# Optimization experiments

Hardware: AMD Instinct MI355X
Metric: run time of the kernel (lower is better)

The kernel has to match this reference:

```python
import jax, jax.numpy as jnp
import numpy as np

N_ATOMS = 16384
N_EDGES = 65536
ATOM_DIM = 29
BOND_DIM = 8
UNITS = 64          # message_units / embed_dim
STEPS = 4
HEADS = 8
DENSE = 512
B_MOL = 256         # molecules
T_ATOMS = 64        # atoms per molecule (N_ATOMS = B_MOL * T_ATOMS)


def setup_inputs() -> dict:
    key = jax.random.key(0)
    ks = jax.random.split(key, 24)
    D = UNITS

    atom_features = jax.random.normal(ks[0], (N_ATOMS, ATOM_DIM), jnp.float32)
    bond_features = jax.random.normal(ks[1], (N_EDGES, BOND_DIM), jnp.float32)
    # edges within molecules
    mol = jax.random.randint(ks[2], (N_EDGES,), 0, B_MOL)
    a = jax.random.randint(ks[3], (N_EDGES,), 0, T_ATOMS)
    b = jax.random.randint(ks[4], (N_EDGES,), 0, T_ATOMS)
    pair_indices = jnp.stack([mol * T_ATOMS + a, mol * T_ATOMS + b], axis=1).astype(jnp.int32)
    molecule_indicator = (jnp.arange(N_ATOMS) // T_ATOMS).astype(jnp.int32)

    def xavier(k, shape, fan_in):
        return jax.random.normal(k, shape, jnp.float32) * (1.0 / np.sqrt(fan_in))

    params = dict(
        kernel=xavier(ks[5], (BOND_DIM, D * D), BOND_DIM),
        kernel_bias=jnp.zeros((D * D,), jnp.float32),
        gru_w_ih=xavier(ks[6], (3 * D, D), D),
        gru_w_hh=xavier(ks[7], (3 * D, D), D),
        gru_b_ih=jnp.zeros((3 * D,), jnp.float32),
        gru_b_hh=jnp.zeros((3 * D,), jnp.float32),
        in_proj_w=xavier(ks[8], (3 * D, D), D),
        in_proj_b=jnp.zeros((3 * D,), jnp.float32),
        out_proj_w=xavier(ks[9], (D, D), D),
        out_proj_b=jnp.zeros((D,), jnp.float32),
        ffn_w1=xavier(ks[10], (D, DENSE), D),
        ffn_b1=jnp.zeros((DENSE,), jnp.float32),
        ffn_w2=xavier(ks[11], (DENSE, D), DENSE),
        ffn_b2=jnp.zeros((D,), jnp.float32),
        ln1_g=jnp.ones((D,), jnp.float32),
        ln1_b=jnp.zeros((D,), jnp.float32),
        ln2_g=jnp.ones((D,), jnp.float32),
        ln2_b=jnp.zeros((D,), jnp.float32),
        d1_w=xavier(ks[12], (D, DENSE), D),
        d1_b=jnp.zeros((DENSE,), jnp.float32),
        d2_w=xavier(ks[13], (DENSE, 1), DENSE),
        d2_b=jnp.zeros((1,), jnp.float32),
    )
    return dict(atom_features=atom_features, bond_features=bond_features,
                pair_indices=pair_indices, molecule_indicator=molecule_indicator, **params)


def _layernorm(x, g, b, eps=1e-5):
    mu = x.mean(-1, keepdims=True)
    var = ((x - mu) ** 2).mean(-1, keepdims=True)
    return (x - mu) * jax.lax.rsqrt(var + eps) * g + b


def _forward(atom_features, bond_features, pair_indices, molecule_indicator,
             kernel, kernel_bias, gru_w_ih, gru_w_hh, gru_b_ih, gru_b_hh,
             in_proj_w, in_proj_b, out_proj_w, out_proj_b,
             ffn_w1, ffn_b1, ffn_w2, ffn_b2, ln1_g, ln1_b, ln2_g, ln2_b,
             d1_w, d1_b, d2_w, d2_b):
    D = UNITS
    n = atom_features.shape[0]
    # pad atom features to message_units
    h = jnp.pad(atom_features, ((0, 0), (0, D - atom_features.shape[1])))

    src = pair_indices[:, 0]
    dst = pair_indices[:, 1]
    # per-edge bond-conditioned transform matrices: [E, D, D]
    bond_mat = (bond_features @ kernel + kernel_bias).reshape(-1, D, D)

    for _ in range(STEPS):
        nbr = h[dst]                                      # gather [E, D]
        msg = jnp.einsum('eij,ej->ei', bond_mat, nbr)     # per-edge matvec
        agg = jax.ops.segment_sum(msg, src, num_segments=n)  # scatter-add [N, D]
        # GRUCell(input=agg, hidden=h)
        gi = agg @ gru_w_ih.T + gru_b_ih
        gh = h @ gru_w_hh.T + gru_b_hh
        i_r, i_z, i_n = jnp.split(gi, 3, axis=-1)
        h_r, h_z, h_n = jnp.split(gh, 3, axis=-1)
        r = jax.nn.sigmoid(i_r + h_r)
        z = jax.nn.sigmoid(i_z + h_z)
        nn_ = jnp.tanh(i_n + r * h_n)
        h = (1.0 - z) * nn_ + z * h

    # PartitionPadding: scatter atoms into [B_MOL, T_ATOMS, D] (indicator sorted, contiguous)
    starts = jnp.searchsorted(molecule_indicator, jnp.arange(B_MOL, dtype=molecule_indicator.dtype))
    pos = jnp.arange(n) - starts[molecule_indicator]
    x = jnp.zeros((B_MOL, T_ATOMS, D), h.dtype).at[molecule_indicator, pos].set(h)

    valid = jnp.any(x != 0, axis=-1)                      # [B, T] key-padding mask

    # multi-head self-attention
    qkv = x @ in_proj_w.T + in_proj_b                     # [B, T, 3D]
    q, k, v = jnp.split(qkv, 3, axis=-1)
    hd = D // HEADS
    q = q.reshape(B_MOL, T_ATOMS, HEADS, hd)
    k = k.reshape(B_MOL, T_ATOMS, HEADS, hd)
    v = v.reshape(B_MOL, T_ATOMS, HEADS, hd)
    scores = jnp.einsum('bqhd,bkhd->bhqk', q, k) / np.sqrt(hd)
    scores = jnp.where(valid[:, None, None, :], scores, -1e9)
    attn = jax.nn.softmax(scores, axis=-1)
    ao = jnp.einsum('bhqk,bkhd->bqhd', attn, v).reshape(B_MOL, T_ATOMS, D)
    ao = ao @ out_proj_w.T + out_proj_b

    y1 = _layernorm(x + ao, ln1_g, ln1_b)
    ffn = jax.nn.relu(y1 @ ffn_w1 + ffn_b1) @ ffn_w2 + ffn_b2
    y2 = _layernorm(y1 + ffn, ln2_g, ln2_b)
    pooled = y2.mean(axis=1)                              # [B, D]

    out = jax.nn.relu(pooled @ d1_w + d1_b)
    return jax.nn.sigmoid(out @ d2_w + d2_b)              # [B, 1]


def reference(atom_features, bond_features, pair_indices, molecule_indicator,
              kernel, kernel_bias, gru_w_ih, gru_w_hh, gru_b_ih, gru_b_hh,
              in_proj_w, in_proj_b, out_proj_w, out_proj_b,
              ffn_w1, ffn_b1, ffn_w2, ffn_b2, ln1_g, ln1_b, ln2_g, ln2_b,
              d1_w, d1_b, d2_w, d2_b):
    return _forward(atom_features, bond_features, pair_indices, molecule_indicator,
                    kernel, kernel_bias, gru_w_ih, gru_w_hh, gru_b_ih, gru_b_hh,
                    in_proj_w, in_proj_b, out_proj_w, out_proj_b,
                    ffn_w1, ffn_b1, ffn_w2, ffn_b2, ln1_g, ln1_b, ln2_g, ln2_b,
                    d1_w, d1_b, d2_w, d2_b)
```

## Files before the change

kernel.cpp:

```cpp
#include <hip/hip_runtime.h>
#include <hip/hip_bf16.h>
#include <math.h>

#define NA 16384
#define NE 65536
#define AD 29

typedef __attribute__((ext_vector_type(8))) short bfrag8;
typedef __attribute__((ext_vector_type(4))) float f32x4;

__device__ __forceinline__ float sigmoidf_(float x) { return 1.0f / (1.0f + expf(-x)); }
__device__ __forceinline__ unsigned short bf16bits(float x) {
  __hip_bfloat16 hb = __float2bfloat16(x);
  return *reinterpret_cast<unsigned short*>(&hb);
}
__device__ __forceinline__ float bf16val(unsigned short u) {
  unsigned int b = ((unsigned int)u) << 16;
  return __uint_as_float(b);
}

__global__ void k_init_prep(
    const float* __restrict__ af, float* __restrict__ h, int* __restrict__ count,
    const float* __restrict__ kern, const float* __restrict__ kbias,
    const float* __restrict__ wih, const float* __restrict__ whh,
    const float* __restrict__ w1, const float* __restrict__ w2,
    const float* __restrict__ ipw, const float* __restrict__ opw,
    unsigned short* __restrict__ KrA,
    unsigned short* __restrict__ Wh, unsigned short* __restrict__ Wl,
    unsigned short* __restrict__ W1h, unsigned short* __restrict__ W1l,
    unsigned short* __restrict__ W2h, unsigned short* __restrict__ W2l,
    unsigned short* __restrict__ PQh, unsigned short* __restrict__ PQl,
    unsigned short* __restrict__ POh, unsigned short* __restrict__ POl) {
  int idx0 = blockIdx.x * 256 + threadIdx.x;
  if (idx0 >= NA * 64) return;
  if (idx0 < NA) count[idx0] = 0;
  {
    int a = idx0 >> 6, d = idx0 & 63;
    h[idx0] = (d < AD) ? af[a * AD + d] : 0.0f;
  }
  if (idx0 < 36864) {
    int idx = idx0;
    int r = idx & 7;
    int lane = (idx >> 3) & 63;
    int tmp2 = idx >> 9;
    int ks = tmp2 % 18, w = tmp2 / 18;
    int i = w * 16 + (lane & 15);
    int kj = ks * 32 + ((lane >> 4) << 3) + r;
    int k9 = kj >> 6, j = kj & 63;
    float v = (k9 < 8) ? kern[k9 * 4096 + i * 64 + j] : kbias[i * 64 + j];
    KrA[idx] = bf16bits(v);
  } else if (idx0 < 61440) {
    int idx = idx0 - 36864;
    int r = idx & 7;
    int lane = (idx >> 3) & 63;
    int t2 = idx >> 9;
    int ks = t2 & 1;
    int t3 = t2 >> 1;
    int q = t3 % 6, w = t3 / 6;
    int s = q / 3, g = q % 3;
    int R = g * 64 + w * 16 + (lane & 15);
    int kk = ks * 32 + ((lane >> 4) << 3) + r;
    float v = (s == 0) ? wih[R * 64 + kk] : whh[R * 64 + kk];
    unsigned short hi = bf16bits(v);
    Wh[idx] = hi;
    Wl[idx] = bf16bits(v - bf16val(hi));
  } else if (idx0 < 126976) {
    int idx = idx0 - 61440;
    int r = idx & 7;
    int lane = (idx >> 3) & 63;
    int rest = (idx >> 9) & 63;
    if (idx < 32768) {
      int tile = rest >> 1, ks = rest & 1;
      int hid = tile * 16 + (lane & 15);
      int kk = ks * 32 + ((lane >> 4) << 3) + r;
      float v = w1[kk * 512 + hid];
      unsigned short hi = bf16bits(v);
      W1h[idx] = hi;
      W1l[idx] = bf16bits(v - bf16val(hi));
    } else {
      int i2 = idx - 32768;
      int tile = rest >> 4, ks = rest & 15;
      int outr = tile * 16 + (lane & 15);
      int kk = ks * 32 + ((lane >> 4) << 3) + r;
      float v = w2[kk * 64 + outr];
      unsigned short hi = bf16bits(v);
      W2h[i2] = hi;
      W2l[i2] = bf16bits(v - bf16val(hi));
    }
  } else if (idx0 < 143360) {
    int i = idx0 - 126976;
    if (i < 12288) {
      int r = i & 7;
      int lane = (i >> 3) & 63;
      int rest = i >> 9;
      int t = rest >> 1, ks = rest & 1;
      int R = t * 16 + (lane & 15);
      int kk = ks * 32 + ((lane >> 4) << 3) + r;
      float v = ipw[R * 64 + kk];
      unsigned short hi = bf16bits(v);
      PQh[i] = hi;
      PQl[i] = bf16bits(v - bf16val(hi));
    } else {
      int i2 = i - 12288;
      int r = i2 & 7;
      int lane = (i2 >> 3) & 63;
      int rest = i2 >> 9;
      int t = rest >> 1, ks = rest & 1;
      int R = t * 16 + (lane & 15);
      int kk = ks * 32 + ((lane >> 4) << 3) + r;
      float v = opw[R * 64 + kk];
      unsigned short hi = bf16bits(v);
      POh[i2] = hi;
      POl[i2] = bf16bits(v - bf16val(hi));
    }
  }
}

__global__ void k_count(const int* __restrict__ pairs, int* __restrict__ count) {
  int e = blockIdx.x * 256 + threadIdx.x;
  if (e >= NE) return;
  atomicAdd(&count[pairs[2 * e]], 1);
}
__global__ void k_scan1(const int* __restrict__ count, int* __restrict__ bsum) {
  __shared__ int red[256];
  int b = blockIdx.x, t = threadIdx.x;
  red[t] = count[b * 256 + t];
  __syncthreads();
  for (int s = 128; s > 0; s >>= 1) { if (t < s) red[t] += red[t + s]; __syncthreads(); }
  if (t == 0) bsum[b] = red[0];
}
__global__ void k_scan2(const int* __restrict__ count, const int* __restrict__ bsum,
                        int* __restrict__ start, int* __restrict__ cursor) {
  __shared__ int sc[256];
  __shared__ int basev;
  int b = blockIdx.x, t = threadIdx.x;
  if (t < 64) {
    int v = (t < b) ? bsum[t] : 0;
#pragma unroll
    for (int off = 1; off < 64; off <<= 1) v += __shfl_xor(v, off, 64);
    if (t == 0) basev = v;
  }
  int v = count[b * 256 + t];
  sc[t] = v;
  __syncthreads();
  for (int off = 1; off < 256; off <<= 1) {
    int add = (t >= off) ? sc[t - off] : 0;
    __syncthreads();
    sc[t] += add;
    __syncthreads();
  }
  int excl = sc[t] - v + basev;
  start[b * 256 + t] = excl;
  cursor[b * 256 + t] = excl;
  if (b * 256 + t == NA - 1) start[NA] = excl + v;
}
__global__ void k_place(const int* __restrict__ pairs, int* __restrict__ cursor,
                        const float* __restrict__ bf, int* __restrict__ sdst,
                        float* __restrict__ sbf) {
  int e = blockIdx.x * 256 + threadIdx.x;
  if (e >= NE) return;
  int src = pairs[2 * e], dst = pairs[2 * e + 1];
  int pos = atomicAdd(&cursor[src], 1);
  sdst[pos] = dst;
  const float4* b4 = reinterpret_cast<const float4*>(&bf[e * 8]);
  float4* s4 = reinterpret_cast<float4*>(&sbf[(size_t)pos * 8]);
  s4[0] = b4[0];
  s4[1] = b4[1];
}

#define MW 4
#define MAW 4
__global__ __launch_bounds__(256, 5) void k_msg(
    const float* __restrict__ h_in, const int* __restrict__ start,
    const int* __restrict__ sdst, const float* __restrict__ sbf,
    const unsigned short* __restrict__ KrA,
    const unsigned short* __restrict__ Wh, const unsigned short* __restrict__ Wl,
    const float* __restrict__ bih, const float* __restrict__ bhh,
    float* __restrict__ h_out) {
  __shared__ __align__(16) unsigned short Tb[16 * 584];
  __shared__ __align__(16) unsigned short Xh[16 * 136];
  __shared__ __align__(16) unsigned short Xl[16 * 136];
  __shared__ __align__(16) float Hf[16 * 68];
  float* AHa = reinterpret_cast<float*>(Tb);
  const int tid = threadIdx.x, lane = tid & 63, wv = tid >> 6;
  const int ablk = blockIdx.x * 16;
  const int awave = ablk + wv * MAW;

#pragma unroll
  for (int aa = 0; aa < MAW; ++aa) {
    const int a = wv * MAW + aa;
    const float v = h_in[(ablk + a) * 64 + lane];
    Hf[a * 68 + lane] = v;
    const unsigned short hi = bf16bits(v);
    Xh[a * 136 + 64 + lane] = hi;
    Xl[a * 136 + 64 + lane] = bf16bits(v - bf16val(hi));
  }

  int s0[MAW], s1[MAW];
#pragma unroll
  for (int a = 0; a < MAW; ++a) {
    s0[a] = __builtin_amdgcn_readfirstlane(start[awave + a]);
    s1[a] = __builtin_amdgcn_readfirstlane(start[awave + a + 1]);
  }
  float t[MAW][9];
#pragma unroll
  for (int a = 0; a < MAW; ++a)
#pragma unroll
    for (int k = 0; k < 9; ++k) t[a][k] = 0.f;

  float hv[MAW][8];
#pragma unroll
  for (int a = 0; a < MAW; ++a) {
    const int cnt = s1[a] - s0[a];
#pragma unroll
    for (int i = 0; i < 8; ++i) {
      hv[a][i] = 0.f;
      if (i < cnt) {
        int d = sdst[s0[a] + i];
        hv[a][i] = h_in[d * 64 + lane];
      }
    }
  }
#pragma unroll
  for (int a = 0; a < MAW; ++a) {
    const int cnt = s1[a] - s0[a];
#pragma unroll
    for (int i = 0; i < 8; ++i) {
      if (i < cnt) {
#pragma unroll
        for (int k = 0; k < 8; ++k)
          t[a][k] = fmaf(sbf[(size_t)(s0[a] + i) * 8 + k], hv[a][i], t[a][k]);
        t[a][8] += hv[a][i];
      }
    }
  }
#pragma unroll
  for (int a = 0; a < MAW; ++a) {
    for (int base = s0[a] + 8; base < s1[a]; base += 8) {
      const int nb = s1[a] - base;
      float hv2[8];
#pragma unroll
      for (int i = 0; i < 8; ++i) {
        hv2[i] = 0.f;
        if (i < nb) {
          int d = sdst[base + i];
          hv2[i] = h_in[d * 64 + lane];
        }
      }
#pragma unroll
      for (int i = 0; i < 8; ++i) {
        if (i < nb) {
#pragma unroll
          for (int k = 0; k < 8; ++k)
            t[a][k] = fmaf(sbf[(size_t)(base + i) * 8 + k], hv2[i], t[a][k]);
          t[a][8] += hv2[i];
        }
      }
    }
  }
#pragma unroll
  for (int a = 0; a < MAW; ++a) {
    const int row = wv * MAW + a;
#pragma unroll
    for (int k = 0; k < 9; ++k) Tb[row * 584 + k * 64 + lane] = bf16bits(t[a][k]);
  }
  __syncthreads();

  f32x4 acc = {0.f, 0.f, 0.f, 0.f};
  const bfrag8* KrA8 = reinterpret_cast<const bfrag8*>(KrA);
  const int tb_base = (lane & 15) * 584 + ((lane >> 4) << 3);
#pragma unroll 3
  for (int ks = 0; ks < 18; ++ks) {
    bfrag8 af = KrA8[(wv * 18 + ks) * 64 + lane];
    bfrag8 bfr = *reinterpret_cast<const bfrag8*>(&Tb[tb_base + ks * 32]);
    acc = __builtin_amdgcn_mfma_f32_16x16x32_bf16(af, bfr, acc, 0, 0, 0);
  }
#pragma unroll
  for (int reg = 0; reg < 4; ++reg) {
    const int ii = wv * 16 + ((lane >> 4) << 2) + reg;
    const unsigned short hi = bf16bits(acc[reg]);
    Xh[(lane & 15) * 136 + ii] = hi;
    Xl[(lane & 15) * 136 + ii] = bf16bits(acc[reg] - bf16val(hi));
  }
  __syncthreads();

  const bfrag8* Wh8 = reinterpret_cast<const bfrag8*>(Wh);
  const bfrag8* Wl8 = reinterpret_cast<const bfrag8*>(Wl);
  f32x4 g0 = {0,0,0,0}, g1 = {0,0,0,0}, g2 = {0,0,0,0};
  f32x4 g3 = {0,0,0,0}, g4 = {0,0,0,0}, g5 = {0,0,0,0};
  f32x4* gptr[6] = {&g0, &g1, &g2, &g3, &g4, &g5};
#pragma unroll
  for (int q = 0; q < 6; ++q) {
    const int s = q / 3;
    f32x4 g = *gptr[q];
#pragma unroll
    for (int ks = 0; ks < 2; ++ks) {
      const int fidx = ((wv * 6 + q) * 2 + ks) * 64 + lane;
      bfrag8 Ah = Wh8[fidx];
      bfrag8 Al = Wl8[fidx];
      const int xoff = (lane & 15) * 136 + (s * 2 + ks) * 32 + ((lane >> 4) << 3);
      bfrag8 Bh = *reinterpret_cast<const bfrag8*>(&Xh[xoff]);
      bfrag8 Bl = *reinterpret_cast<const bfrag8*>(&Xl[xoff]);
      g = __builtin_amdgcn_mfma_f32_16x16x32_bf16(Ah, Bh, g, 0, 0, 0);
      g = __builtin_amdgcn_mfma_f32_16x16x32_bf16(Ah, Bl, g, 0, 0, 0);
      g = __builtin_amdgcn_mfma_f32_16x16x32_bf16(Al, Bh, g, 0, 0, 0);
    }
    *gptr[q] = g;
  }
  const int ib = wv * 16 + ((lane >> 4) << 2);
  const float4 bir4 = *reinterpret_cast<const float4*>(&bih[ib]);
  const float4 biz4 = *reinterpret_cast<const float4*>(&bih[64 + ib]);
  const float4 bin4 = *reinterpret_cast<const float4*>(&bih[128 + ib]);
  const float4 bhr4 = *reinterpret_cast<const float4*>(&bhh[ib]);
  const float4 bhz4 = *reinterpret_cast<const float4*>(&bhh[64 + ib]);
  const float4 bhn4 = *reinterpret_cast<const float4*>(&bhh[128 + ib]);
  const float birA[4] = {bir4.x, bir4.y, bir4.z, bir4.w};
  const float bizA[4] = {biz4.x, biz4.y, biz4.z, biz4.w};
  const float binA[4] = {bin4.x, bin4.y, bin4.z, bin4.w};
  const float bhrA[4] = {bhr4.x, bhr4.y, bhr4.z, bhr4.w};
  const float bhzA[4] = {bhz4.x, bhz4.y, bhz4.z, bhz4.w};
  const float bhnA[4] = {bhn4.x, bhn4.y, bhn4.z, bhn4.w};
#pragma unroll
  for (int reg = 0; reg < 4; ++reg) {
    const int i = ib + reg;
    const int atom = lane & 15;
    const float r = sigmoidf_(g0[reg] + birA[reg] + g3[reg] + bhrA[reg]);
    const float z = sigmoidf_(g1[reg] + bizA[reg] + g4[reg] + bhzA[reg]);
    const float nn = tanhf(g2[reg] + binA[reg] + r * (g5[reg] + bhnA[reg]));
    const float hold = Hf[atom * 68 + i];
    AHa[atom * 68 + i] = (1.0f - z) * nn + z * hold;
  }
  __syncthreads();
#pragma unroll
  for (int aa = 0; aa < MAW; ++aa) {
    const int a = wv * MAW + aa;
    h_out[(ablk + a) * 64 + lane] = AHa[a * 68 + lane];
  }
}

__global__ __launch_bounds__(256, 1) void k_mol(
    const float* __restrict__ h,
    const unsigned short* __restrict__ PQh, const unsigned short* __restrict__ PQl,
    const unsigned short* __restrict__ POh, const unsigned short* __restrict__ POl,
    const float* __restrict__ ipb, const float* __restrict__ opb,
    const float* __restrict__ l1g, const float* __restrict__ l1b,
    float* __restrict__ y1) {
  __shared__ __align__(16) float Hf[64 * 65];
  __shared__ __align__(16) unsigned short Xh[64 * 72];
  __shared__ __align__(16) unsigned short Xl[64 * 72];
  __shared__ __align__(16) float QKVs[192 * 65];
  __shared__ __align__(16) unsigned short AOh[64 * 72];
  __shared__ __align__(16) unsigned short AOl[64 * 72];
  __shared__ __align__(16) float Of[64 * 65];
  __shared__ int vd[64];
  const int tid = threadIdx.x, lane = tid & 63, wv = tid >> 6;
  const int mol = blockIdx.x;

  for (int aa = 0; aa < 16; ++aa) {
    const int a = wv * 16 + aa;
    const float v = h[(mol * 64 + a) * 64 + lane];
    Hf[a * 65 + lane] = v;
    const unsigned short hi = bf16bits(v);
    Xh[a * 72 + lane] = hi;
    Xl[a * 72 + lane] = bf16bits(v - bf16val(hi));
    int nz = __any(v != 0.0f);
    if (lane == 0) vd[a] = nz;
  }
  __syncthreads();

  const bfrag8* PQh8 = reinterpret_cast<const bfrag8*>(PQh);
  const bfrag8* PQl8 = reinterpret_cast<const bfrag8*>(PQl);
  const int xoff_b = (wv * 16 + (lane & 15)) * 72 + ((lane >> 4) << 3);
#pragma unroll 3
  for (int tile = 0; tile < 12; ++tile) {
    f32x4 acc = {0.f, 0.f, 0.f, 0.f};
#pragma unroll
    for (int ks = 0; ks < 2; ++ks) {
      const int fidx = (tile * 2 + ks) * 64 + lane;
      bfrag8 Ah = PQh8[fidx];
      bfrag8 Al = PQl8[fidx];
      bfrag8 Bh = *reinterpret_cast<const bfrag8*>(&Xh[xoff_b + ks * 32]);
      bfrag8 Bl = *reinterpret_cast<const bfrag8*>(&Xl[xoff_b + ks * 32]);
      acc = __builtin_amdgcn_mfma_f32_16x16x32_bf16(Ah, Bh, acc, 0, 0, 0);
      acc = __builtin_amdgcn_mfma_f32_16x16x32_bf16(Ah, Bl, acc, 0, 0, 0);
      acc = __builtin_amdgcn_mfma_f32_16x16x32_bf16(Al, Bh, acc, 0, 0, 0);
    }
#pragma unroll
    for (int reg = 0; reg < 4; ++reg) {
      const int row = tile * 16 + ((lane >> 4) << 2) + reg;
      QKVs[row * 65 + wv * 16 + (lane & 15)] = acc[reg] + ipb[row];
    }
  }
  __syncthreads();

#pragma unroll
  for (int hp = 0; hp < 2; ++hp) {
    const int hh = wv * 2 + hp;
    float q[8];
#pragma unroll
    for (int j = 0; j < 8; ++j) q[j] = QKVs[(hh * 8 + j) * 65 + lane];
    float m = -3.0e38f, l = 0.f, o[8] = {0,0,0,0,0,0,0,0};
    for (int t = 0; t < 64; ++t) {
      float s = 0.f;
#pragma unroll
      for (int j = 0; j < 8; ++j) s += q[j] * QKVs[(64 + hh * 8 + j) * 65 + t];
      s *= 0.35355339059327373f;
      s = vd[t] ? s : -1.0e9f;
      float mn = fmaxf(m, s);
      float c = expf(m - mn);
      float p = expf(s - mn);
      l = l * c + p;
#pragma unroll
      for (int j = 0; j < 8; ++j) o[j] = o[j] * c + p * QKVs[(128 + hh * 8 + j) * 65 + t];
      m = mn;
    }
    const float inv = 1.0f / l;
#pragma unroll
    for (int j = 0; j < 8; ++j) {
      const float v = o[j] * inv;
      const unsigned short hi = bf16bits(v);
      AOh[lane * 72 + hh * 8 + j] = hi;
      AOl[lane * 72 + hh * 8 + j] = bf16bits(v - bf16val(hi));
    }
  }
  __syncthreads();

  const bfrag8* POh8 = reinterpret_cast<const bfrag8*>(POh);
  const bfrag8* POl8 = reinterpret_cast<const bfrag8*>(POl);
  const int aoff_b = (wv * 16 + (lane & 15)) * 72 + ((lane >> 4) << 3);
#pragma unroll
  for (int tile = 0; tile < 4; ++tile) {
    f32x4 acc = {0.f, 0.f, 0.f, 0.f};
#pragma unroll
    for (int ks = 0; ks < 2; ++ks) {
      const int fidx = (tile * 2 + ks) * 64 + lane;
      bfrag8 Ah = POh8[fidx];
      bfrag8 Al = POl8[fidx];
      bfrag8 Bh = *reinterpret_cast<const bfrag8*>(&AOh[aoff_b + ks * 32]);
      bfrag8 Bl = *reinterpret_cast<const bfrag8*>(&AOl[aoff_b + ks * 32]);
      acc = __builtin_amdgcn_mfma_f32_16x16x32_bf16(Ah, Bh, acc, 0, 0, 0);
      acc = __builtin_amdgcn_mfma_f32_16x16x32_bf16(Ah, Bl, acc, 0, 0, 0);
      acc = __builtin_amdgcn_mfma_f32_16x16x32_bf16(Al, Bh, acc, 0, 0, 0);
    }
#pragma unroll
    for (int reg = 0; reg < 4; ++reg) {
      const int dim = tile * 16 + ((lane >> 4) << 2) + reg;
      Of[(wv * 16 + (lane & 15)) * 65 + dim] = acc[reg] + opb[dim];
    }
  }
  __syncthreads();

  const float gg = l1g[lane], bbb = l1b[lane];
  for (int aa = 0; aa < 16; ++aa) {
    const int a = wv * 16 + aa;
    float val = Hf[a * 65 + lane] + Of[a * 65 + lane];
    float s1 = val, s2 = val * val;
#pragma unroll
    for (int mm = 1; mm < 64; mm <<= 1) {
      s1 += __shfl_xor(s1, mm, 64);
      s2 += __shfl_xor(s2, mm, 64);
    }
    float mu = s1 * 0.015625f;
    float var = s2 * 0.015625f - mu * mu;
    y1[(mol * 64 + a) * 64 + lane] = (val - mu) * rsqrtf(var + 1e-5f) * gg + bbb;
  }
}

__global__ __launch_bounds__(256, 3) void k_ffn(
    const float* __restrict__ y1,
    const unsigned short* __restrict__ W1h, const unsigned short* __restrict__ W1l,
    const unsigned short* __restrict__ W2h, const unsigned short* __restrict__ W2l,
    const float* __restrict__ b1, const float* __restrict__ b2,
    const float* __restrict__ g, const float* __restrict__ bb,
    float* __restrict__ y2) {
  __shared__ __align__(16) unsigned short Xh[16 * 72];
  __shared__ __align__(16) unsigned short Xl[16 * 72];
  __shared__ __align__(16) unsigned short Hh[16 * 520];
  __shared__ __align__(16) unsigned short Hl[16 * 520];
  __shared__ __align__(16) float Y1f[16 * 68];
  __shared__ __align__(16) float Of[16 * 68];
  const int tid = threadIdx.x, lane = tid & 63, wv = tid >> 6;
  const int ablk = blockIdx.x * 16;

#pragma unroll
  for (int aa = 0; aa < 4; ++aa) {
    const int a = wv * 4 + aa;
    const float v = y1[(ablk + a) * 64 + lane];
    Y1f[a * 68 + lane] = v;
    const unsigned short hi = bf16bits(v);
    Xh[a * 72 + lane] = hi;
    Xl[a * 72 + lane] = bf16bits(v - bf16val(hi));
  }
  __syncthreads();

  const bfrag8* W1h8 = reinterpret_cast<const bfrag8*>(W1h);
  const bfrag8* W1l8 = reinterpret_cast<const bfrag8*>(W1l);
  const int xoff_base = (lane & 15) * 72 + ((lane >> 4) << 3);
#pragma unroll 2
  for (int t = 0; t < 8; ++t) {
    f32x4 acc = {0.f, 0.f, 0.f, 0.f};
    const int tile = wv * 8 + t;
#pragma unroll
    for (int ks = 0; ks < 2; ++ks) {
      const int fidx = (tile * 2 + ks) * 64 + lane;
      bfrag8 Ah = W1h8[fidx];
      bfrag8 Al = W1l8[fidx];
      bfrag8 Bh = *reinterpret_cast<const bfrag8*>(&Xh[xoff_base + ks * 32]);
      bfrag8 Bl = *reinterpret_cast<const bfrag8*>(&Xl[xoff_base + ks * 32]);
      acc = __builtin_amdgcn_mfma_f32_16x16x32_bf16(Ah, Bh, acc, 0, 0, 0);
      acc = __builtin_amdgcn_mfma_f32_16x16x32_bf16(Ah, Bl, acc, 0, 0, 0);
      acc = __builtin_amdgcn_mfma_f32_16x16x32_bf16(Al, Bh, acc, 0, 0, 0);
    }
#pragma unroll
    for (int reg = 0; reg < 4; ++reg) {
      const int hid = tile * 16 + ((lane >> 4) << 2) + reg;
      float val = fmaxf(acc[reg] + b1[hid], 0.f);
      const unsigned short hi = bf16bits(val);
      Hh[(lane & 15) * 520 + hid] = hi;
      Hl[(lane & 15) * 520 + hid] = bf16bits(val - bf16val(hi));
    }
  }
  __syncthreads();

  const bfrag8* W2h8 = reinterpret_cast<const bfrag8*>(W2h);
  const bfrag8* W2l8 = reinterpret_cast<const bfrag8*>(W2l);
  f32x4 acc2 = {0.f, 0.f, 0.f, 0.f};
  const int hoff_base = (lane & 15) * 520 + ((lane >> 4) << 3);
#pragma unroll 4
  for (int ks = 0; ks < 16; ++ks) {
    const int fidx = (wv * 16 + ks) * 64 + lane;
    bfrag8 Ah = W2h8[fidx];
    bfrag8 Al = W2l8[fidx];
    bfrag8 Bh = *reinterpret_cast<const bfrag8*>(&Hh[hoff_base + ks * 32]);
    bfrag8 Bl = *reinterpret_cast<const bfrag8*>(&Hl[hoff_base + ks * 32]);
    acc2 = __builtin_amdgcn_mfma_f32_16x16x32_bf16(Ah, Bh, acc2, 0, 0, 0);
    acc2 = __builtin_amdgcn_mfma_f32_16x16x32_bf16(Ah, Bl, acc2, 0, 0, 0);
    acc2 = __builtin_amdgcn_mfma_f32_16x16x32_bf16(Al, Bh, acc2, 0, 0, 0);
  }
#pragma unroll
  for (int reg = 0; reg < 4; ++reg) {
    const int outr = wv * 16 + ((lane >> 4) << 2) + reg;
    Of[(lane & 15) * 68 + outr] = acc2[reg] + b2[outr];
  }
  __syncthreads();

  const float gg = g[lane], bbb = bb[lane];
#pragma unroll
  for (int aa = 0; aa < 4; ++aa) {
    const int a = wv * 4 + aa;
    float val = Y1f[a * 68 + lane] + Of[a * 68 + lane];
    float s1 = val, s2 = val * val;
#pragma unroll
    for (int mm = 1; mm < 64; mm <<= 1) {
      s1 += __shfl_xor(s1, mm, 64);
      s2 += __shfl_xor(s2, mm, 64);
    }
    float mu = s1 * 0.015625f;
    float var = s2 * 0.015625f - mu * mu;
    y2[(ablk + a) * 64 + lane] = (val - mu) * rsqrtf(var + 1e-5f) * gg + bbb;
  }
}

__global__ __launch_bounds__(256) void k_head(
    const float* __restrict__ y2, const float* __restrict__ d1w,
    const float* __restrict__ d1b, const float* __restrict__ d2w,
    const float* __restrict__ d2b, float* __restrict__ out) {
  const int b = blockIdx.x;
  const int tid = threadIdx.x, lane = tid & 63, wv = tid >> 6;
  __shared__ float part[4][64];
  __shared__ float p_s[64];
  __shared__ float red_s[4];
  float s = 0.f;
#pragma unroll 4
  for (int t = wv * 16; t < wv * 16 + 16; ++t) s += y2[(b * 64 + t) * 64 + lane];
  part[wv][lane] = s;
  __syncthreads();
  if (tid < 64)
    p_s[tid] = (part[0][tid] + part[1][tid] + part[2][tid] + part[3][tid]) * 0.015625f;
  __syncthreads();
  float acc = 0.f;
#pragma unroll
  for (int rep = 0; rep < 2; ++rep) {
    int c = rep * 256 + tid;
    float hvv = d1b[c];
    for (int d = 0; d < 64; ++d) hvv += p_s[d] * d1w[d * 512 + c];
    acc += fmaxf(hvv, 0.f) * d2w[c];
  }
#pragma unroll
  for (int mm = 1; mm < 64; mm <<= 1) acc += __shfl_xor(acc, mm, 64);
  if ((tid & 63) == 0) red_s[tid >> 6] = acc;
  __syncthreads();
  if (tid == 0) {
    float t = red_s[0] + red_s[1] + red_s[2] + red_s[3] + d2b[0];
    out[b] = 1.0f / (1.0f + expf(-t));
  }
}

extern "C" void kernel_launch(void* const* d_in, const int* in_sizes, int n_in,
                              void* d_out, int out_size, void* d_ws, size_t ws_size,
                              hipStream_t stream) {
  (void)in_sizes; (void)n_in; (void)out_size; (void)ws_size;
  const float* af   = (const float*)d_in[0];
  const float* bfeat= (const float*)d_in[1];
  const int*   pairs= (const int*)d_in[2];
  const float* kern = (const float*)d_in[4];
  const float* kbias= (const float*)d_in[5];
  const float* wih  = (const float*)d_in[6];
  const float* whh  = (const float*)d_in[7];
  const float* bih  = (const float*)d_in[8];
  const float* bhh  = (const float*)d_in[9];
  const float* ipw  = (const float*)d_in[10];
  const float* ipb  = (const float*)d_in[11];
  const float* opw  = (const float*)d_in[12];
  const float* opb  = (const float*)d_in[13];
  const float* fw1  = (const float*)d_in[14];
  const float* fb1  = (const float*)d_in[15];
  const float* fw2  = (const float*)d_in[16];
  const float* fb2  = (const float*)d_in[17];
  const float* l1g  = (const float*)d_in[18];
  const float* l1b  = (const float*)d_in[19];
  const float* l2g  = (const float*)d_in[20];
  const float* l2b  = (const float*)d_in[21];
  const float* d1w  = (const float*)d_in[22];
  const float* d1b  = (const float*)d_in[23];
  const float* d2w  = (const float*)d_in[24];
  const float* d2b  = (const float*)d_in[25];
  float* out = (float*)d_out;

  float* ws = (float*)d_ws;
  float* h      = ws;
  float* h2     = h + (size_t)NA * 64;
  float* qkv    = h2 + (size_t)NA * 64;
  float* ao     = qkv + (size_t)NA * 192;
  float* y1     = ao + (size_t)NA * 64;
  float* y2     = y1 + (size_t)NA * 64;
  float* pooled = y2 + (size_t)NA * 64;
  int*   valid  = (int*)(pooled + 256 * 64);
  (void)ao; (void)pooled;

  unsigned short* W1h = (unsigned short*)(valid + NA);
  unsigned short* W1l = W1h + 32768;
  unsigned short* W2h = W1l + 32768;
  unsigned short* W2l = W2h + 32768;
  unsigned short* PQh = W2l + 32768;
  unsigned short* PQl = PQh + 12288;
  unsigned short* POh = PQl + 12288;
  unsigned short* POl = POh + 4096;

  unsigned short* KrA = (unsigned short*)qkv;
  int*   count  = (int*)(qkv + 36864);
  int*   start  = count + NA;
  int*   cursor = start + NA + 1;
  int*   bsum   = cursor + NA;
  int*   sdst   = bsum + 256;
  float* sbf    = (float*)(sdst + NE + 8);
  unsigned short* Wh = (unsigned short*)(sbf + (size_t)NE * 8 + 64);
  unsigned short* Wl = Wh + 24576;

  k_init_prep<<<NA * 64 / 256, 256, 0, stream>>>(
      af, h, count, kern, kbias, wih, whh, fw1, fw2, ipw, opw,
      KrA, Wh, Wl, W1h, W1l, W2h, W2l, PQh, PQl, POh, POl);
  k_count<<<NE / 256, 256, 0, stream>>>(pairs, count);
  k_scan1<<<64, 256, 0, stream>>>(count, bsum);
  k_scan2<<<64, 256, 0, stream>>>(count, bsum, start, cursor);
  k_place<<<NE / 256, 256, 0, stream>>>(pairs, cursor, bfeat, sdst, sbf);

  float* hin = h;
  float* hout = h2;
  for (int s = 0; s < 4; ++s) {
    k_msg<<<NA / 16, 256, 0, stream>>>(hin, start, sdst, sbf, KrA,
                                       Wh, Wl, bih, bhh, hout);
    float* tmp = hin; hin = hout; hout = tmp;
  }

  k_mol<<<256, 256, 0, stream>>>(h, PQh, PQl, POh, POl, ipb, opb, l1g, l1b, y1);
  k_ffn<<<NA / 16, 256, 0, stream>>>(y1, W1h, W1l, W2h, W2l, fb1, fb2, l2g, l2b, y2);
  k_head<<<256, 256, 0, stream>>>(y2, d1w, d1b, d2w, d2b, out);
}
```

Baseline: 153.8 us.

## Fuse four message-passing steps into one per-molecule kernel with LDS-resident state

Replaces the four per-step k_msg launches with one k_mp kernel that runs one block per molecule. The block keeps all 64 atom states in shared memory across the four steps, so neighbor gathers read LDS instead of global memory. This relies on every edge staying inside its molecule, which the task builds in by construction. It removes the extra launches and the global h round trips between steps. In exchange the grid shrinks to 256 blocks with one block per CU, and each wave now serially processes 16 atoms, which lowers parallelism and latency hiding.

After: 338.7 us. 2.2x slower.

```diff
diff --git a/kernel.cpp b/kernel.cpp
--- a/kernel.cpp
+++ b/kernel.cpp
@@ -168,173 +168,187 @@
   s4[1] = b4[1];
 }
 
-#define MW 4
-#define MAW 4
-__global__ __launch_bounds__(256, 5) void k_msg(
+__global__ __launch_bounds__(256, 1) void k_mp(
     const float* __restrict__ h_in, const int* __restrict__ start,
     const int* __restrict__ sdst, const float* __restrict__ sbf,
     const unsigned short* __restrict__ KrA,
     const unsigned short* __restrict__ Wh, const unsigned short* __restrict__ Wl,
     const float* __restrict__ bih, const float* __restrict__ bhh,
     float* __restrict__ h_out) {
-  __shared__ __align__(16) unsigned short Tb[16 * 584];
-  __shared__ __align__(16) unsigned short Xh[16 * 136];
-  __shared__ __align__(16) unsigned short Xl[16 * 136];
-  __shared__ __align__(16) float Hf[16 * 68];
+  __shared__ __align__(16) unsigned short Tb[64 * 584];
+  __shared__ __align__(16) unsigned short Xh[64 * 136];
+  __shared__ __align__(16) unsigned short Xl[64 * 136];
+  __shared__ __align__(16) float Hf[64 * 68];
   float* AHa = reinterpret_cast<float*>(Tb);
   const int tid = threadIdx.x, lane = tid & 63, wv = tid >> 6;
-  const int ablk = blockIdx.x * 16;
-  const int awave = ablk + wv * MAW;
-
-#pragma unroll
-  for (int aa = 0; aa < MAW; ++aa) {
-    const int a = wv * MAW + aa;
-    const float v = h_in[(ablk + a) * 64 + lane];
+  const int mol = blockIdx.x;
+  const int molbase = mol * 64;
+
+#pragma unroll
+  for (int aa = 0; aa < 16; ++aa) {
+    const int a = wv * 16 + aa;
+    const float v = h_in[(molbase + a) * 64 + lane];
     Hf[a * 68 + lane] = v;
     const unsigned short hi = bf16bits(v);
     Xh[a * 136 + 64 + lane] = hi;
     Xl[a * 136 + 64 + lane] = bf16bits(v - bf16val(hi));
   }
-
-  int s0[MAW], s1[MAW];
-#pragma unroll
-  for (int a = 0; a < MAW; ++a) {
-    s0[a] = __builtin_amdgcn_readfirstlane(start[awave + a]);
-    s1[a] = __builtin_amdgcn_readfirstlane(start[awave + a + 1]);
-  }
-  float t[MAW][9];
-#pragma unroll
-  for (int a = 0; a < MAW; ++a)
-#pragma unroll
-    for (int k = 0; k < 9; ++k) t[a][k] = 0.f;
-
-  float hv[MAW][8];
-#pragma unroll
-  for (int a = 0; a < MAW; ++a) {
-    const int cnt = s1[a] - s0[a];
-#pragma unroll
-    for (int i = 0; i < 8; ++i) {
-      hv[a][i] = 0.f;
-      if (i < cnt) {
-        int d = sdst[s0[a] + i];
-        hv[a][i] = h_in[d * 64 + lane];
-      }
-    }
-  }
-#pragma unroll
-  for (int a = 0; a < MAW; ++a) {
-    const int cnt = s1[a] - s0[a];
-#pragma unroll
-    for (int i = 0; i < 8; ++i) {
-      if (i < cnt) {
-#pragma unroll
-        for (int k = 0; k < 8; ++k)
-          t[a][k] = fmaf(sbf[(size_t)(s0[a] + i) * 8 + k], hv[a][i], t[a][k]);
-        t[a][8] += hv[a][i];
-      }
-    }
-  }
-#pragma unroll
-  for (int a = 0; a < MAW; ++a) {
-    for (int base = s0[a] + 8; base < s1[a]; base += 8) {
-      const int nb = s1[a] - base;
-      float hv2[8];
-#pragma unroll
-      for (int i = 0; i < 8; ++i) {
-        hv2[i] = 0.f;
-        if (i < nb) {
-          int d = sdst[base + i];
-          hv2[i] = h_in[d * 64 + lane];
-        }
-      }
-#pragma unroll
-      for (int i = 0; i < 8; ++i) {
-        if (i < nb) {
-#pragma unroll
-          for (int k = 0; k < 8; ++k)
-            t[a][k] = fmaf(sbf[(size_t)(base + i) * 8 + k], hv2[i], t[a][k]);
-          t[a][8] += hv2[i];
-        }
-      }
-    }
-  }
-#pragma unroll
-  for (int a = 0; a < MAW; ++a) {
-    const int row = wv * MAW + a;
-#pragma unroll
-    for (int k = 0; k < 9; ++k) Tb[row * 584 + k * 64 + lane] = bf16bits(t[a][k]);
-  }
-  __syncthreads();
-
-  f32x4 acc = {0.f, 0.f, 0.f, 0.f};
+  const int bb = (lane <= 16) ? start[molbase + wv * 16 + lane] : 0;
+  __syncthreads();
+
   const bfrag8* KrA8 = reinterpret_cast<const bfrag8*>(KrA);
-  const int tb_base = (lane & 15) * 584 + ((lane >> 4) << 3);
-#pragma unroll 3
-  for (int ks = 0; ks < 18; ++ks) {
-    bfrag8 af = KrA8[(wv * 18 + ks) * 64 + lane];
-    bfrag8 bfr = *reinterpret_cast<const bfrag8*>(&Tb[tb_base + ks * 32]);
-    acc = __builtin_amdgcn_mfma_f32_16x16x32_bf16(af, bfr, acc, 0, 0, 0);
-  }
-#pragma unroll
-  for (int reg = 0; reg < 4; ++reg) {
-    const int ii = wv * 16 + ((lane >> 4) << 2) + reg;
-    const unsigned short hi = bf16bits(acc[reg]);
-    Xh[(lane & 15) * 136 + ii] = hi;
-    Xl[(lane & 15) * 136 + ii] = bf16bits(acc[reg] - bf16val(hi));
-  }
-  __syncthreads();
-
   const bfrag8* Wh8 = reinterpret_cast<const bfrag8*>(Wh);
   const bfrag8* Wl8 = reinterpret_cast<const bfrag8*>(Wl);
-  f32x4 g0 = {0,0,0,0}, g1 = {0,0,0,0}, g2 = {0,0,0,0};
-  f32x4 g3 = {0,0,0,0}, g4 = {0,0,0,0}, g5 = {0,0,0,0};
-  f32x4* gptr[6] = {&g0, &g1, &g2, &g3, &g4, &g5};
-#pragma unroll
-  for (int q = 0; q < 6; ++q) {
-    const int s = q / 3;
-    f32x4 g = *gptr[q];
-#pragma unroll
-    for (int ks = 0; ks < 2; ++ks) {
-      const int fidx = ((wv * 6 + q) * 2 + ks) * 64 + lane;
-      bfrag8 Ah = Wh8[fidx];
-      bfrag8 Al = Wl8[fidx];
-      const int xoff = (lane & 15) * 136 + (s * 2 + ks) * 32 + ((lane >> 4) << 3);
-      bfrag8 Bh = *reinterpret_cast<const bfrag8*>(&Xh[xoff]);
-      bfrag8 Bl = *reinterpret_cast<const bfrag8*>(&Xl[xoff]);
-      g = __builtin_amdgcn_mfma_f32_16x16x32_bf16(Ah, Bh, g, 0, 0, 0);
-      g = __builtin_amdgcn_mfma_f32_16x16x32_bf16(Ah, Bl, g, 0, 0, 0);
-      g = __builtin_amdgcn_mfma_f32_16x16x32_bf16(Al, Bh, g, 0, 0, 0);
-    }
-    *gptr[q] = g;
-  }
-  const int ib = wv * 16 + ((lane >> 4) << 2);
-  const float4 bir4 = *reinterpret_cast<const float4*>(&bih[ib]);
-  const float4 biz4 = *reinterpret_cast<const float4*>(&bih[64 + ib]);
-  const float4 bin4 = *reinterpret_cast<const float4*>(&bih[128 + ib]);
-  const float4 bhr4 = *reinterpret_cast<const float4*>(&bhh[ib]);
-  const float4 bhz4 = *reinterpret_cast<const float4*>(&bhh[64 + ib]);
-  const float4 bhn4 = *reinterpret_cast<const float4*>(&bhh[128 + ib]);
-  const float birA[4] = {bir4.x, bir4.y, bir4.z, bir4.w};
-  const float bizA[4] = {biz4.x, biz4.y, biz4.z, biz4.w};
-  const float binA[4] = {bin4.x, bin4.y, bin4.z, bin4.w};
-  const float bhrA[4] = {bhr4.x, bhr4.y, bhr4.z, bhr4.w};
-  const float bhzA[4] = {bhz4.x, bhz4.y, bhz4.z, bhz4.w};
-  const float bhnA[4] = {bhn4.x, bhn4.y, bhn4.z, bhn4.w};
-#pragma unroll
-  for (int reg = 0; reg < 4; ++reg) {
-    const int i = ib + reg;
-    const int atom = lane & 15;
-    const float r = sigmoidf_(g0[reg] + birA[reg] + g3[reg] + bhrA[reg]);
-    const float z = sigmoidf_(g1[reg] + bizA[reg] + g4[reg] + bhzA[reg]);
-    const float nn = tanhf(g2[reg] + binA[reg] + r * (g5[reg] + bhnA[reg]));
-    const float hold = Hf[atom * 68 + i];
-    AHa[atom * 68 + i] = (1.0f - z) * nn + z * hold;
-  }
-  __syncthreads();
-#pragma unroll
-  for (int aa = 0; aa < MAW; ++aa) {
-    const int a = wv * MAW + aa;
-    h_out[(ablk + a) * 64 + lane] = AHa[a * 68 + lane];
+  const int atomg = wv * 16 + (lane & 15);
+
+  for (int step = 0; step < 4; ++step) {
+#pragma unroll
+    for (int g = 0; g < 4; ++g) {
+      int s0[4], s1[4];
+#pragma unroll
+      for (int aa = 0; aa < 4; ++aa) {
+        s0[aa] = __shfl(bb, g * 4 + aa, 64);
+        s1[aa] = __shfl(bb, g * 4 + aa + 1, 64);
+      }
+      float t[4][9];
+#pragma unroll
+      for (int aa = 0; aa < 4; ++aa)
+#pragma unroll
+        for (int k = 0; k < 9; ++k) t[aa][k] = 0.f;
+      float hv[4][8];
+#pragma unroll
+      for (int aa = 0; aa < 4; ++aa) {
+        const int cnt = s1[aa] - s0[aa];
+#pragma unroll
+        for (int i = 0; i < 8; ++i) {
+          hv[aa][i] = 0.f;
+          if (i < cnt) {
+            int dloc = sdst[s0[aa] + i] - molbase;
+            hv[aa][i] = Hf[dloc * 68 + lane];
+          }
+        }
+      }
+#pragma unroll
+      for (int aa = 0; aa < 4; ++aa) {
+        const int cnt = s1[aa] - s0[aa];
+#pragma unroll
+        for (int i = 0; i < 8; ++i) {
+          if (i < cnt) {
+#pragma unroll
+            for (int k = 0; k < 8; ++k)
+              t[aa][k] = fmaf(sbf[(size_t)(s0[aa] + i) * 8 + k], hv[aa][i], t[aa][k]);
+            t[aa][8] += hv[aa][i];
+          }
+        }
+      }
+#pragma unroll
+      for (int aa = 0; aa < 4; ++aa) {
+        for (int base = s0[aa] + 8; base < s1[aa]; base += 8) {
+          const int nb = s1[aa] - base;
+#pragma unroll
+          for (int i = 0; i < 8; ++i) {
+            if (i < nb) {
+              int dloc = sdst[base + i] - molbase;
+              float hvv = Hf[dloc * 68 + lane];
+#pragma unroll
+              for (int k = 0; k < 8; ++k)
+                t[aa][k] = fmaf(sbf[(size_t)(base + i) * 8 + k], hvv, t[aa][k]);
+              t[aa][8] += hvv;
+            }
+          }
+        }
+      }
+#pragma unroll
+      for (int aa = 0; aa < 4; ++aa) {
+        const int row = wv * 16 + g * 4 + aa;
+#pragma unroll
+        for (int k = 0; k < 9; ++k) Tb[row * 584 + k * 64 + lane] = bf16bits(t[aa][k]);
+      }
+    }
+
+    const int tb_base = atomg * 584 + ((lane >> 4) << 3);
+#pragma unroll
+    for (int ic = 0; ic < 4; ++ic) {
+      f32x4 acc = {0.f, 0.f, 0.f, 0.f};
+#pragma unroll 3
+      for (int ks = 0; ks < 18; ++ks) {
+        bfrag8 af = KrA8[(ic * 18 + ks) * 64 + lane];
+        bfrag8 bfr = *reinterpret_cast<const bfrag8*>(&Tb[tb_base + ks * 32]);
+        acc = __builtin_amdgcn_mfma_f32_16x16x32_bf16(af, bfr, acc, 0, 0, 0);
+      }
+#pragma unroll
+      for (int reg = 0; reg < 4; ++reg) {
+        const int ii = ic * 16 + ((lane >> 4) << 2) + reg;
+        const unsigned short hi = bf16bits(acc[reg]);
+        Xh[atomg * 136 + ii] = hi;
+        Xl[atomg * 136 + ii] = bf16bits(acc[reg] - bf16val(hi));
+      }
+    }
+    __syncthreads();
+
+#pragma unroll
+    for (int ic = 0; ic < 4; ++ic) {
+      f32x4 g0 = {0,0,0,0}, g1 = {0,0,0,0}, g2 = {0,0,0,0};
+      f32x4 g3 = {0,0,0,0}, g4 = {0,0,0,0}, g5 = {0,0,0,0};
+      f32x4* gptr[6] = {&g0, &g1, &g2, &g3, &g4, &g5};
+#pragma unroll
+      for (int q = 0; q < 6; ++q) {
+        const int s = q / 3;
+        f32x4 g = *gptr[q];
+#pragma unroll
+        for (int ks = 0; ks < 2; ++ks) {
+          const int fidx = ((ic * 6 + q) * 2 + ks) * 64 + lane;
+          bfrag8 Ah = Wh8[fidx];
+          bfrag8 Al = Wl8[fidx];
+          const int xoff = atomg * 136 + (s * 2 + ks) * 32 + ((lane >> 4) << 3);
+          bfrag8 Bh = *reinterpret_cast<const bfrag8*>(&Xh[xoff]);
+          bfrag8 Bl = *reinterpret_cast<const bfrag8*>(&Xl[xoff]);
+          g = __builtin_amdgcn_mfma_f32_16x16x32_bf16(Ah, Bh, g, 0, 0, 0);
+          g = __builtin_amdgcn_mfma_f32_16x16x32_bf16(Ah, Bl, g, 0, 0, 0);
+          g = __builtin_amdgcn_mfma_f32_16x16x32_bf16(Al, Bh, g, 0, 0, 0);
+        }
+        *gptr[q] = g;
+      }
+      const int ib = ic * 16 + ((lane >> 4) << 2);
+      const float4 bir4 = *reinterpret_cast<const float4*>(&bih[ib]);
+      const float4 biz4 = *reinterpret_cast<const float4*>(&bih[64 + ib]);
+      const float4 bin4 = *reinterpret_cast<const float4*>(&bih[128 + ib]);
+      const float4 bhr4 = *reinterpret_cast<const float4*>(&bhh[ib]);
+      const float4 bhz4 = *reinterpret_cast<const float4*>(&bhh[64 + ib]);
+      const float4 bhn4 = *reinterpret_cast<const float4*>(&bhh[128 + ib]);
+      const float birA[4] = {bir4.x, bir4.y, bir4.z, bir4.w};
+      const float bizA[4] = {biz4.x, biz4.y, biz4.z, biz4.w};
+      const float binA[4] = {bin4.x, bin4.y, bin4.z, bin4.w};
+      const float bhrA[4] = {bhr4.x, bhr4.y, bhr4.z, bhr4.w};
+      const float bhzA[4] = {bhz4.x, bhz4.y, bhz4.z, bhz4.w};
+      const float bhnA[4] = {bhn4.x, bhn4.y, bhn4.z, bhn4.w};
+#pragma unroll
+      for (int reg = 0; reg < 4; ++reg) {
+        const int i = ib + reg;
+        const float r = sigmoidf_(g0[reg] + birA[reg] + g3[reg] + bhrA[reg]);
+        const float z = sigmoidf_(g1[reg] + bizA[reg] + g4[reg] + bhzA[reg]);
+        const float nn = tanhf(g2[reg] + binA[reg] + r * (g5[reg] + bhnA[reg]));
+        const float hold = Hf[atomg * 68 + i];
+        AHa[atomg * 68 + i] = (1.0f - z) * nn + z * hold;
+      }
+    }
+
+#pragma unroll
+    for (int aa = 0; aa < 16; ++aa) {
+      const int a = wv * 16 + aa;
+      const float v = AHa[a * 68 + lane];
+      Hf[a * 68 + lane] = v;
+      const unsigned short hi = bf16bits(v);
+      Xh[a * 136 + 64 + lane] = hi;
+      Xl[a * 136 + 64 + lane] = bf16bits(v - bf16val(hi));
+    }
+    __syncthreads();
+  }
+
+#pragma unroll
+  for (int aa = 0; aa < 16; ++aa) {
+    const int a = wv * 16 + aa;
+    h_out[(molbase + a) * 64 + lane] = Hf[a * 68 + lane];
   }
 }
 
@@ -665,13 +679,7 @@
   k_scan2<<<64, 256, 0, stream>>>(count, bsum, start, cursor);
   k_place<<<NE / 256, 256, 0, stream>>>(pairs, cursor, bfeat, sdst, sbf);
 
-  float* hin = h;
-  float* hout = h2;
-  for (int s = 0; s < 4; ++s) {
-    k_msg<<<NA / 16, 256, 0, stream>>>(hin, start, sdst, sbf, KrA,
-                                       Wh, Wl, bih, bhh, hout);
-    float* tmp = hin; hin = hout; hout = tmp;
-  }
+  k_mp<<<256, 256, 0, stream>>>(h, start, sdst, sbf, KrA, Wh, Wl, bih, bhh, h);
 
   k_mol<<<256, 256, 0, stream>>>(h, PQh, PQl, POh, POl, ipb, opb, l1g, l1b, y1);
   k_ffn<<<NA / 16, 256, 0, stream>>>(y1, W1h, W1l, W2h, W2l, fb1, fb2, l2g, l2b, y2);
```
